# Kernel tuning notes

Hardware: AMD Instinct MI355X
Metric: run time of the kernel (lower is better)

## Reference

```python
import jax, jax.numpy as jnp
import numpy as np

INPUT, HIDDEN, CLASSES = 4096, 4096, 1000


def setup_inputs() -> dict:
    key = jax.random.key(0)
    kx, kw1, kb1, kw2, kb2 = jax.random.split(key, 5)
    return {
        "x": jax.random.normal(kx, (8192, INPUT), dtype=jnp.float32),
        "fc1_weight": jax.random.normal(kw1, (HIDDEN, INPUT), dtype=jnp.float32),
        "fc1_bias": jax.random.normal(kb1, (HIDDEN,), dtype=jnp.float32),
        "fc2_weight": jax.random.normal(kw2, (CLASSES, HIDDEN), dtype=jnp.float32),
        "fc2_bias": jax.random.normal(kb2, (CLASSES,), dtype=jnp.float32),
    }


def reference(x, fc1_weight, fc1_bias, fc2_weight, fc2_bias):
    # x: [B, INPUT] (module flattens; already flat here)
    hidden = jnp.einsum("bi,hi->bh", x, fc1_weight) + fc1_bias  # [B, H]
    activated = jax.nn.relu(hidden)
    logits = jnp.einsum("bh,ch->bc", activated, fc2_weight) + fc2_bias  # [B, C]
    return jax.nn.softmax(logits, axis=-1)
```

## Files before the change

### kernel.cpp

```cpp
#include <hip/hip_runtime.h>
#include <hip/hip_fp16.h>
#include <stdint.h>

typedef __attribute__((ext_vector_type(8))) _Float16 f16x8;
typedef __attribute__((ext_vector_type(4))) _Float16 f16x4;
typedef __attribute__((ext_vector_type(4))) float f32x4;

__device__ __forceinline__ void split4(const f32x4 v, f16x4 &h, f16x4 &l) {
    #pragma unroll
    for (int i = 0; i < 4; ++i) {
        float a = v[i];
        _Float16 hh = (_Float16)a;
        h[i] = hh;
        l[i] = (_Float16)(a - (float)hh);
    }
}

__global__ __launch_bounds__(256)
void split_rows(const float* __restrict__ src, _Float16* __restrict__ h,
                _Float16* __restrict__ l, int srcRows, long long total4)
{
    const long long stride = (long long)gridDim.x * blockDim.x;
    for (long long i = (long long)blockIdx.x * blockDim.x + threadIdx.x; i < total4; i += stride) {
        const long long e = i << 2;
        const int row = (int)(e >> 12);
        f16x4 hv = {}, lv = {};
        if (row < srcRows) {
            f32x4 v = *(const f32x4*)(src + e);
            split4(v, hv, lv);
        }
        *(f16x4*)(h + e) = hv;
        *(f16x4*)(l + e) = lv;
    }
}


#define BARRIER() __builtin_amdgcn_s_barrier()
#define LGKM0() do { asm volatile("s_waitcnt lgkmcnt(0)" ::: "memory"); __builtin_amdgcn_sched_barrier(0); } while (0)

template<int N> __device__ __forceinline__ void VMCNT() {
    asm volatile("s_waitcnt vmcnt(%0)" :: "n"(N) : "memory");
    __builtin_amdgcn_sched_barrier(0);
}

__device__ __forceinline__ void gload16(const _Float16* g, _Float16* l) {
    __builtin_amdgcn_global_load_lds(
        (const __attribute__((address_space(1))) void*)g,
        (__attribute__((address_space(3))) void*)l, 16, 0, 0);
}

template<int MI, bool SPLITOUT>
__global__ __launch_bounds__(512, 2)
void gemm3_phase(const _Float16* __restrict__ Agh, const _Float16* __restrict__ Agl,
                 const _Float16* __restrict__ Bgh, const _Float16* __restrict__ Bgl,
                 const float* __restrict__ bias,
                 _Float16* __restrict__ Oh, _Float16* __restrict__ Ol,
                 float* __restrict__ Of, int ldo, int Nstore,
                 int K, int nBM)
{
    extern __shared__ _Float16 lds[];
    constexpr int WROWS = MI * 16;
    constexpr int BM    = MI * 32;
    constexpr int CHA   = MI * 2;
    constexpr int PW    = (2*CHA + 32) / 8;
    constexpr int NA    = PW - 4;
    constexpr int ALO   = CHA * 512;
    constexpr int BHO   = 2 * CHA * 512;
    constexpr int BUFS  = 2*CHA*512 + 16384;

    const int tid  = threadIdx.x;
    const int lane = tid & 63;
    const int wave = tid >> 6;
    const int wm = wave >> 2;
    const int wn = wave & 3;
    const int fr = lane & 15;
    const int fg = lane >> 4;

    const int nwg  = gridDim.x;
    const int cpx  = nwg >> 3;
    const int orig = blockIdx.x;
    const int swzb = (orig & 7) * cpx + (orig >> 3);
    const int bm = swzb % nBM;
    const int bn = swzb / nBM;
    const int m0 = bm * BM;
    const int n0 = bn * 256;

    const _Float16* gptr[8];
    int loff[8];
    #pragma unroll
    for (int i = 0; i < PW; ++i) {
        int p, q;
        if (i < NA) {
            const int j = wave * NA + i;
            p = j / CHA; q = j % CHA;
        } else {
            const int ni = i - NA;
            q = ni + (wave & 3) * 4;
            p = 2 + (wave >> 2);
        }
        const int row = q*16 + (lane >> 2);
        const int gc  = (lane & 3) ^ ((row >> 1) & 3);
        const _Float16* plane = (p == 0) ? Agh : (p == 1) ? Agl : (p == 2) ? Bgh : Bgl;
        const size_t grow = (size_t)((p < 2) ? m0 : n0) + row;
        gptr[i] = plane + grow * (size_t)K + gc * 8;
        loff[i] = ((p < 2) ? p * ALO : BHO + (p - 2) * 8192) + q * 512;
    }

    const int swz8 = (fg ^ ((fr >> 1) & 3)) * 8;
    int aoff[MI], boff[4];
    #pragma unroll
    for (int mi = 0; mi < MI; ++mi) aoff[mi] = (wm*WROWS + mi*16 + fr)*32 + swz8;
    #pragma unroll
    for (int ni = 0; ni < 4; ++ni)  boff[ni] = BHO + (wn*64 + ni*16 + fr)*32 + swz8;

    f32x4 acc[MI][4] = {};

    #pragma unroll
    for (int i = 0; i < PW; ++i) { gload16(gptr[i], &lds[loff[i]]); gptr[i] += 32; }
    VMCNT<3>(); BARRIER();

    const int NT = K >> 5;
    int bb = 0;

#define PH(NI, IB, IE, WAIT) do {                                                     \
        bhf = *(const f16x8*)&lds[bb + boff[NI]];                                     \
        blf = *(const f16x8*)&lds[bb + 8192 + boff[NI]];                              \
        _Pragma("unroll")                                                             \
        for (int i = (IB); i < (IE); ++i) {                                           \
            gload16(gptr[i], &lds[nb + loff[i]]); gptr[i] += 32;                      \
        }                                                                             \
        BARRIER(); LGKM0();                                                           \
        __builtin_amdgcn_s_setprio(1);                                                \
        _Pragma("unroll")                                                             \
        for (int mi = 0; mi < MI; ++mi) {                                             \
            acc[mi][NI] = __builtin_amdgcn_mfma_f32_16x16x32_f16(ah[mi], bhf, acc[mi][NI], 0, 0, 0); \
            acc[mi][NI] = __builtin_amdgcn_mfma_f32_16x16x32_f16(ah[mi], blf, acc[mi][NI], 0, 0, 0); \
            acc[mi][NI] = __builtin_amdgcn_mfma_f32_16x16x32_f16(al[mi], bhf, acc[mi][NI], 0, 0, 0); \
        }                                                                             \
        __builtin_amdgcn_s_setprio(0);                                                \
        WAIT;                                                                         \
        BARRIER();                                                                    \
    } while (0)

    for (int t = 0; t < NT - 1; ++t) {
        const int nb = BUFS - bb;
        f16x8 ah[MI], al[MI], bhf, blf;
        #pragma unroll
        for (int mi = 0; mi < MI; ++mi) {
            ah[mi] = *(const f16x8*)&lds[bb + aoff[mi]];
            al[mi] = *(const f16x8*)&lds[bb + ALO + aoff[mi]];
        }
        PH(0, 0,    NA,   VMCNT<PW-2>());
        PH(1, NA,   NA+2, VMCNT<PW-1>());
        PH(2, NA+2, PW,   VMCNT<PW>());
        PH(3, 0,    0,    VMCNT<3>());
        bb = nb;
    }
    {
        const int nb = BUFS - bb;
        f16x8 ah[MI], al[MI], bhf, blf;
        #pragma unroll
        for (int mi = 0; mi < MI; ++mi) {
            ah[mi] = *(const f16x8*)&lds[bb + aoff[mi]];
            al[mi] = *(const f16x8*)&lds[bb + ALO + aoff[mi]];
        }
        PH(0, 0, 0, VMCNT<2>());
        PH(1, 0, 0, VMCNT<1>());
        PH(2, 0, 0, VMCNT<0>());
        PH(3, 0, 0, );
        (void)nb;
    }
#undef PH

    #pragma unroll
    for (int ni = 0; ni < 4; ++ni) {
        const int n = n0 + wn*64 + ni*16 + fr;
        if (!SPLITOUT && n >= Nstore) continue;
        const float bv = bias[n];
        #pragma unroll
        for (int mi = 0; mi < MI; ++mi) {
            #pragma unroll
            for (int j = 0; j < 4; ++j) {
                const int m = m0 + wm*WROWS + mi*16 + fg*4 + j;
                float v = acc[mi][ni][j] + bv;
                if (SPLITOUT) {
                    v = fmaxf(v, 0.f);
                    const _Float16 hh = (_Float16)v;
                    Oh[(size_t)m * ldo + n] = hh;
                    Ol[(size_t)m * ldo + n] = (_Float16)(v - (float)hh);
                } else {
                    Of[(size_t)m * ldo + n] = v;
                }
            }
        }
    }
}

#define TILE_M 128
#define TILE_N 128
#define TILE_K 32
#define LDSK   40

template<bool RELU, bool NGUARD>
__global__ __launch_bounds__(256, 2)
void gemm_split3(const float* __restrict__ A, const float* __restrict__ B,
                 const float* __restrict__ bias, float* __restrict__ C,
                 int K, int ldc, int Nreal)
{
    __shared__ _Float16 Ah[TILE_M][LDSK];
    __shared__ _Float16 Al[TILE_M][LDSK];
    __shared__ _Float16 Bh[TILE_N][LDSK];
    __shared__ _Float16 Bl[TILE_N][LDSK];

    const int tid  = threadIdx.x;
    const int lane = tid & 63;
    const int wave = tid >> 6;
    const int wr   = wave >> 1;
    const int wc   = wave & 1;
    const int m0   = blockIdx.x * TILE_M;
    const int n0   = blockIdx.y * TILE_N;
    const int srow = tid >> 3;
    const int scol = (tid & 7) << 2;
    const int fr = lane & 15;
    const int fg = lane >> 4;

    f32x4 acc[4][4] = {};

    for (int kt = 0; kt < K; kt += TILE_K) {
        __syncthreads();
        #pragma unroll
        for (int p = 0; p < 4; ++p) {
            const int row = srow + p * 32;
            f32x4 v = *(const f32x4*)(A + (size_t)(m0 + row) * K + kt + scol);
            f16x4 hv, lv;
            split4(v, hv, lv);
            *(f16x4*)&Ah[row][scol] = hv;
            *(f16x4*)&Al[row][scol] = lv;
        }
        #pragma unroll
        for (int p = 0; p < 4; ++p) {
            const int row = srow + p * 32;
            f32x4 v = {0.f, 0.f, 0.f, 0.f};
            if (!NGUARD || (n0 + row) < Nreal)
                v = *(const f32x4*)(B + (size_t)(n0 + row) * K + kt + scol);
            f16x4 hv, lv;
            split4(v, hv, lv);
            *(f16x4*)&Bh[row][scol] = hv;
            *(f16x4*)&Bl[row][scol] = lv;
        }
        __syncthreads();

        f16x8 ah[4], al[4];
        #pragma unroll
        for (int mi = 0; mi < 4; ++mi) {
            const int r = wr * 64 + mi * 16 + fr;
            ah[mi] = *(const f16x8*)&Ah[r][fg * 8];
            al[mi] = *(const f16x8*)&Al[r][fg * 8];
        }
        #pragma unroll
        for (int ni = 0; ni < 4; ++ni) {
            const int r = wc * 64 + ni * 16 + fr;
            const f16x8 bh = *(const f16x8*)&Bh[r][fg * 8];
            const f16x8 bl = *(const f16x8*)&Bl[r][fg * 8];
            #pragma unroll
            for (int mi = 0; mi < 4; ++mi) {
                acc[mi][ni] = __builtin_amdgcn_mfma_f32_16x16x32_f16(ah[mi], bh, acc[mi][ni], 0, 0, 0);
                acc[mi][ni] = __builtin_amdgcn_mfma_f32_16x16x32_f16(ah[mi], bl, acc[mi][ni], 0, 0, 0);
                acc[mi][ni] = __builtin_amdgcn_mfma_f32_16x16x32_f16(al[mi], bh, acc[mi][ni], 0, 0, 0);
            }
        }
    }

    #pragma unroll
    for (int ni = 0; ni < 4; ++ni) {
        const int n = n0 + wc * 64 + ni * 16 + fr;
        if (NGUARD && n >= Nreal) continue;
        const float bv = bias[n];
        #pragma unroll
        for (int mi = 0; mi < 4; ++mi) {
            #pragma unroll
            for (int j = 0; j < 4; ++j) {
                const int m = m0 + wr * 64 + mi * 16 + fg * 4 + j;
                float val = acc[mi][ni][j] + bv;
                if (RELU) val = fmaxf(val, 0.f);
                C[(size_t)m * ldc + n] = val;
            }
        }
    }
}

__global__ __launch_bounds__(256)
void softmax_rows(float* __restrict__ out, int rows, int cols)
{
    const int lane = threadIdx.x & 63;
    const int row  = blockIdx.x * 4 + (threadIdx.x >> 6);
    if (row >= rows) return;
    float* p = out + (size_t)row * cols;

    float v[16];
    float mx = -3.4e38f;
    #pragma unroll
    for (int j = 0; j < 16; ++j) {
        const int c = lane + j * 64;
        v[j] = (c < cols) ? p[c] : -3.4e38f;
        mx = fmaxf(mx, v[j]);
    }
    #pragma unroll
    for (int off = 32; off > 0; off >>= 1)
        mx = fmaxf(mx, __shfl_xor(mx, off));

    float s = 0.f;
    #pragma unroll
    for (int j = 0; j < 16; ++j) {
        const int c = lane + j * 64;
        const float e = (c < cols) ? __expf(v[j] - mx) : 0.f;
        v[j] = e;
        s += e;
    }
    #pragma unroll
    for (int off = 32; off > 0; off >>= 1)
        s += __shfl_xor(s, off);

    const float inv = 1.f / s;
    #pragma unroll
    for (int j = 0; j < 16; ++j) {
        const int c = lane + j * 64;
        if (c < cols) p[c] = v[j] * inv;
    }
}

extern "C" void kernel_launch(void* const* d_in, const int* in_sizes, int n_in,
                              void* d_out, int out_size, void* d_ws, size_t ws_size,
                              hipStream_t stream)
{
    const float* x  = (const float*)d_in[0];
    const float* w1 = (const float*)d_in[1];
    const float* b1 = (const float*)d_in[2];
    const float* w2 = (const float*)d_in[3];
    const float* b2 = (const float*)d_in[4];
    float* out = (float*)d_out;

    const size_t SZ_X  = (size_t)8192 * 4096 * 2;
    const size_t SZ_W1 = (size_t)4096 * 4096 * 2;
    const size_t SZ_W2 = (size_t)1024 * 4096 * 2;

    size_t off = 0;
    auto take = [&](size_t b) { size_t o = off; off += (b + 255) & ~(size_t)255; return o; };
    const size_t o_xh  = take(SZ_X),  o_xl  = take(SZ_X);
    const size_t o_w1h = take(SZ_W1), o_w1l = take(SZ_W1);
    const size_t o_w2h = take(SZ_W2), o_w2l = take(SZ_W2);
    const size_t o_ah  = take(SZ_X),  o_al  = take(SZ_X);
    const size_t need = off;

    bool attr_ok =
        (hipFuncSetAttribute((const void*)gemm3_phase<8, true>,
                             hipFuncAttributeMaxDynamicSharedMemorySize, 131072) == hipSuccess) &&
        (hipFuncSetAttribute((const void*)gemm3_phase<4, false>,
                             hipFuncAttributeMaxDynamicSharedMemorySize, 131072) == hipSuccess);

    const dim3 blk256(256, 1, 1), blk512(512, 1, 1);

    if (attr_ok && ws_size >= need) {
        char* w = (char*)d_ws;
        _Float16 *xh  = (_Float16*)(w + o_xh),  *xl  = (_Float16*)(w + o_xl);
        _Float16 *w1h = (_Float16*)(w + o_w1h), *w1l = (_Float16*)(w + o_w1l);
        _Float16 *w2h = (_Float16*)(w + o_w2h), *w2l = (_Float16*)(w + o_w2l);
        _Float16 *ath = (_Float16*)(w + o_ah),  *atl = (_Float16*)(w + o_al);

        hipLaunchKernelGGL(split_rows, dim3(2048), blk256, 0, stream, x,  xh,  xl,  8192, (long long)8192 * 1024);
        hipLaunchKernelGGL(split_rows, dim3(2048), blk256, 0, stream, w1, w1h, w1l, 4096, (long long)4096 * 1024);
        hipLaunchKernelGGL(split_rows, dim3(1024), blk256, 0, stream, w2, w2h, w2l, 1000, (long long)1024 * 1024);

        hipLaunchKernelGGL((gemm3_phase<8, true>), dim3(512), blk512, 131072, stream,
                           xh, xl, w1h, w1l, b1, ath, atl, (float*)nullptr, 4096, 4096, 4096, 32);
        hipLaunchKernelGGL((gemm3_phase<4, false>), dim3(256), blk512, 98304, stream,
                           ath, atl, w2h, w2l, b2, (_Float16*)nullptr, (_Float16*)nullptr,
                           out, 1000, 1000, 4096, 64);
        hipLaunchKernelGGL(softmax_rows, dim3(2048), blk256, 0, stream, out, 8192, 1000);
    } else {
        float* act = (float*)d_ws;
        hipLaunchKernelGGL((gemm_split3<true, false>), dim3(64, 32), blk256, 0, stream,
                           x, w1, b1, act, 4096, 4096, 4096);
        hipLaunchKernelGGL((gemm_split3<false, true>), dim3(64, 8), blk256, 0, stream,
                           act, w2, b2, out, 4096, 1000, 1000);
        hipLaunchKernelGGL(softmax_rows, dim3(2048), blk256, 0, stream, out, 8192, 1000);
    }
}
```

Baseline: 1.013 ms.

## Restructure GEMM main loop into two half-phases with fewer barriers and chunked tile swizzle

Replaces the four-phase-per-K-tile loop, which had two barriers and an explicit lgkmcnt(0) wait per phase, with two half-phases that each cover two N sub-tiles. This halves the barriers per K step, and A fragments are now read from LDS inside the MFMA loop so the compiler can interleave them, instead of preloading all of them up front. It also adds a chunked block-index mapping for the first GEMM that groups 4 M-tiles per XCD to improve L2 reuse, and relaxes the vmcnt waits. The cost is deeper reliance on compiler scheduling of LDS reads against MFMAs, and possible register-pressure changes.

```diff
diff --git a/kernel.cpp b/kernel.cpp
--- a/kernel.cpp
+++ b/kernel.cpp
@@ -36,7 +36,8 @@
 
 
 #define BARRIER() __builtin_amdgcn_s_barrier()
-#define LGKM0() do { asm volatile("s_waitcnt lgkmcnt(0)" ::: "memory"); __builtin_amdgcn_sched_barrier(0); } while (0)
+#define SB0()     __builtin_amdgcn_sched_barrier(0)
+#define MFMA16    __builtin_amdgcn_mfma_f32_16x16x32_f16
 
 template<int N> __device__ __forceinline__ void VMCNT() {
     asm volatile("s_waitcnt vmcnt(%0)" :: "n"(N) : "memory");
@@ -49,14 +50,14 @@
         (__attribute__((address_space(3))) void*)l, 16, 0, 0);
 }
 
-template<int MI, bool SPLITOUT>
+template<int MI, bool SPLITOUT, bool CHUNKSWZ>
 __global__ __launch_bounds__(512, 2)
-void gemm3_phase(const _Float16* __restrict__ Agh, const _Float16* __restrict__ Agl,
-                 const _Float16* __restrict__ Bgh, const _Float16* __restrict__ Bgl,
-                 const float* __restrict__ bias,
-                 _Float16* __restrict__ Oh, _Float16* __restrict__ Ol,
-                 float* __restrict__ Of, int ldo, int Nstore,
-                 int K, int nBM)
+void gemm3_v5(const _Float16* __restrict__ Agh, const _Float16* __restrict__ Agl,
+              const _Float16* __restrict__ Bgh, const _Float16* __restrict__ Bgl,
+              const float* __restrict__ bias,
+              _Float16* __restrict__ Oh, _Float16* __restrict__ Ol,
+              float* __restrict__ Of, int ldo, int Nstore,
+              int K, int nBM)
 {
     extern __shared__ _Float16 lds[];
     constexpr int WROWS = MI * 16;
@@ -76,12 +77,17 @@
     const int fr = lane & 15;
     const int fg = lane >> 4;
 
-    const int nwg  = gridDim.x;
-    const int cpx  = nwg >> 3;
+    int bm, bn;
     const int orig = blockIdx.x;
-    const int swzb = (orig & 7) * cpx + (orig >> 3);
-    const int bm = swzb % nBM;
-    const int bn = swzb / nBM;
+    if (CHUNKSWZ) {
+        bm = ((orig & 7) << 2) | ((orig >> 3) & 3);
+        bn = orig >> 5;
+    } else {
+        const int cpx  = gridDim.x >> 3;
+        const int swzb = (orig & 7) * cpx + (orig >> 3);
+        bm = swzb % nBM;
+        bn = swzb / nBM;
+    }
     const int m0 = bm * BM;
     const int n0 = bn * 256;
 
@@ -117,60 +123,53 @@
 
     #pragma unroll
     for (int i = 0; i < PW; ++i) { gload16(gptr[i], &lds[loff[i]]); gptr[i] += 32; }
-    VMCNT<3>(); BARRIER();
+    VMCNT<2>(); BARRIER(); SB0();
+
+#define DO_HALF(NIa, NIb, IB, IE, STG)                                        \
+    do {                                                                      \
+        const f16x8 bha = *(const f16x8*)&lds[bb + boff[NIa]];                \
+        const f16x8 bla = *(const f16x8*)&lds[bb + 8192 + boff[NIa]];         \
+        const f16x8 bhb = *(const f16x8*)&lds[bb + boff[NIb]];                \
+        const f16x8 blb = *(const f16x8*)&lds[bb + 8192 + boff[NIb]];         \
+        if (STG) {                                                            \
+            _Pragma("unroll")                                                 \
+            for (int i = (IB); i < (IE); ++i) {                               \
+                gload16(gptr[i], &lds[nb + loff[i]]); gptr[i] += 32;          \
+            }                                                                 \
+        }                                                                     \
+        SB0();                                                                \
+        __builtin_amdgcn_s_setprio(1);                                        \
+        _Pragma("unroll")                                                     \
+        for (int mi = 0; mi < MI; ++mi) {                                     \
+            const f16x8 ah = *(const f16x8*)&lds[bb + aoff[mi]];              \
+            const f16x8 al = *(const f16x8*)&lds[bb + ALO + aoff[mi]];        \
+            acc[mi][NIa] = MFMA16(ah, bha, acc[mi][NIa], 0, 0, 0);            \
+            acc[mi][NIa] = MFMA16(ah, bla, acc[mi][NIa], 0, 0, 0);            \
+            acc[mi][NIa] = MFMA16(al, bha, acc[mi][NIa], 0, 0, 0);            \
+            acc[mi][NIb] = MFMA16(ah, bhb, acc[mi][NIb], 0, 0, 0);            \
+            acc[mi][NIb] = MFMA16(ah, blb, acc[mi][NIb], 0, 0, 0);            \
+            acc[mi][NIb] = MFMA16(al, bhb, acc[mi][NIb], 0, 0, 0);            \
+        }                                                                     \
+        __builtin_amdgcn_s_setprio(0);                                        \
+    } while (0)
 
     const int NT = K >> 5;
     int bb = 0;
-
-#define PH(NI, IB, IE, WAIT) do {                                                     \
-        bhf = *(const f16x8*)&lds[bb + boff[NI]];                                     \
-        blf = *(const f16x8*)&lds[bb + 8192 + boff[NI]];                              \
-        _Pragma("unroll")                                                             \
-        for (int i = (IB); i < (IE); ++i) {                                           \
-            gload16(gptr[i], &lds[nb + loff[i]]); gptr[i] += 32;                      \
-        }                                                                             \
-        BARRIER(); LGKM0();                                                           \
-        __builtin_amdgcn_s_setprio(1);                                                \
-        _Pragma("unroll")                                                             \
-        for (int mi = 0; mi < MI; ++mi) {                                             \
-            acc[mi][NI] = __builtin_amdgcn_mfma_f32_16x16x32_f16(ah[mi], bhf, acc[mi][NI], 0, 0, 0); \
-            acc[mi][NI] = __builtin_amdgcn_mfma_f32_16x16x32_f16(ah[mi], blf, acc[mi][NI], 0, 0, 0); \
-            acc[mi][NI] = __builtin_amdgcn_mfma_f32_16x16x32_f16(al[mi], bhf, acc[mi][NI], 0, 0, 0); \
-        }                                                                             \
-        __builtin_amdgcn_s_setprio(0);                                                \
-        WAIT;                                                                         \
-        BARRIER();                                                                    \
-    } while (0)
-
     for (int t = 0; t < NT - 1; ++t) {
         const int nb = BUFS - bb;
-        f16x8 ah[MI], al[MI], bhf, blf;
-        #pragma unroll
-        for (int mi = 0; mi < MI; ++mi) {
-            ah[mi] = *(const f16x8*)&lds[bb + aoff[mi]];
-            al[mi] = *(const f16x8*)&lds[bb + ALO + aoff[mi]];
-        }
-        PH(0, 0,    NA,   VMCNT<PW-2>());
-        PH(1, NA,   NA+2, VMCNT<PW-1>());
-        PH(2, NA+2, PW,   VMCNT<PW>());
-        PH(3, 0,    0,    VMCNT<3>());
+        DO_HALF(0, 1, 0, NA + 2, true);
+        VMCNT<NA + 2>(); BARRIER(); SB0();
+        DO_HALF(2, 3, NA + 2, PW, true);
+        VMCNT<2>(); BARRIER(); SB0();
         bb = nb;
     }
     {
-        const int nb = BUFS - bb;
-        f16x8 ah[MI], al[MI], bhf, blf;
-        #pragma unroll
-        for (int mi = 0; mi < MI; ++mi) {
-            ah[mi] = *(const f16x8*)&lds[bb + aoff[mi]];
-            al[mi] = *(const f16x8*)&lds[bb + ALO + aoff[mi]];
-        }
-        PH(0, 0, 0, VMCNT<2>());
-        PH(1, 0, 0, VMCNT<1>());
-        PH(2, 0, 0, VMCNT<0>());
-        PH(3, 0, 0, );
-        (void)nb;
-    }
-#undef PH
+        const int nb = 0; (void)nb;
+        DO_HALF(0, 1, 0, 0, false);
+        VMCNT<0>(); BARRIER(); SB0();
+        DO_HALF(2, 3, 0, 0, false);
+    }
+#undef DO_HALF
 
     #pragma unroll
     for (int ni = 0; ni < 4; ++ni) {
@@ -353,9 +352,9 @@
     const size_t need = off;
 
     bool attr_ok =
-        (hipFuncSetAttribute((const void*)gemm3_phase<8, true>,
+        (hipFuncSetAttribute((const void*)gemm3_v5<8, true, true>,
                              hipFuncAttributeMaxDynamicSharedMemorySize, 131072) == hipSuccess) &&
-        (hipFuncSetAttribute((const void*)gemm3_phase<4, false>,
+        (hipFuncSetAttribute((const void*)gemm3_v5<4, false, false>,
                              hipFuncAttributeMaxDynamicSharedMemorySize, 131072) == hipSuccess);
 
     const dim3 blk256(256, 1, 1), blk512(512, 1, 1);
@@ -371,9 +370,9 @@
         hipLaunchKernelGGL(split_rows, dim3(2048), blk256, 0, stream, w1, w1h, w1l, 4096, (long long)4096 * 1024);
         hipLaunchKernelGGL(split_rows, dim3(1024), blk256, 0, stream, w2, w2h, w2l, 1000, (long long)1024 * 1024);
 
-        hipLaunchKernelGGL((gemm3_phase<8, true>), dim3(512), blk512, 131072, stream,
+        hipLaunchKernelGGL((gemm3_v5<8, true, true>), dim3(512), blk512, 131072, stream,
                            xh, xl, w1h, w1l, b1, ath, atl, (float*)nullptr, 4096, 4096, 4096, 32);
-        hipLaunchKernelGGL((gemm3_phase<4, false>), dim3(256), blk512, 98304, stream,
+        hipLaunchKernelGGL((gemm3_v5<4, false, false>), dim3(256), blk512, 98304, stream,
                            ath, atl, w2h, w2l, b2, (_Float16*)nullptr, (_Float16*)nullptr,
                            out, 1000, 1000, 4096, 64);
         hipLaunchKernelGGL(softmax_rows, dim3(2048), blk256, 0, stream, out, 8192, 1000);
```

New measurement: 969.8 us. 1.04x faster.
